# Performance work log

Hardware: AMD Instinct MI355X
Metric: run time of the kernel (lower is better)

Reference implementation:

```python
import jax, jax.numpy as jnp
import numpy as np

EPS = 1e-12


def setup_inputs() -> dict:
    key = jax.random.key(0)
    k1, k2 = jax.random.split(key)
    N, K, D = 32768, 2048, 512
    node_repr = jax.random.normal(k1, (N, D), dtype=jnp.float32)
    mask = jnp.ones((N, 1), dtype=jnp.float32)
    # nn.Embedding weight for the centroids (euclidean branch: exp_map_zero is identity)
    centroid_weight = jax.random.normal(k2, (K, D), dtype=jnp.float32)
    return {"node_repr": node_repr, "mask": mask, "centroid_weight": centroid_weight}


def reference(node_repr, mask, centroid_weight):
    # Euclidean manifold: exp_map_zero(x) = x; distance(x, y) = ||x - y||_2.
    # The torch code expands to [N*K, D]; here we fuse via the Gram-matrix identity
    x2 = jnp.sum(node_repr * node_repr, axis=-1, keepdims=True)        # [N, 1]
    c2 = jnp.sum(centroid_weight * centroid_weight, axis=-1)           # [K]
    xc = jnp.einsum('nd,kd->nk', node_repr, centroid_weight)           # [N, K] GEMM
    d2 = x2 + c2[None, :] - 2.0 * xc                                   # [N, K]
    dist = jnp.sqrt(jnp.maximum(d2, EPS))                              # [N, K]
    node_centroid_dist = dist[None, :, :] * mask[None, :, :]           # [1, N, K] (mask broadcasts [1,N,1])
    graph_centroid_dist = jnp.sum(node_centroid_dist, axis=1) / jnp.sum(mask)  # [1, K]
    return graph_centroid_dist, node_centroid_dist
```

## Files before the change

kernel.cpp:

```cpp
#include <hip/hip_runtime.h>
#include <hip/hip_bf16.h>
#include <math.h>

typedef __bf16 bf16_t;
typedef __bf16 bf16x4 __attribute__((ext_vector_type(4)));
typedef __bf16 bf16x8 __attribute__((ext_vector_type(8)));
typedef float floatx4 __attribute__((ext_vector_type(4)));

#define N_NODES 32768
#define K_CENT  2048
#define D_DIM   512

__global__ void prep_rows_kernel(const float* __restrict__ src,
                                 bf16_t* __restrict__ dst,
                                 float* __restrict__ sq) {
  const int w = threadIdx.x >> 6;
  const int l = threadIdx.x & 63;
  const int row = blockIdx.x * 4 + w;
  const float4* s = (const float4*)(src + (size_t)row * D_DIM);
  float4 f0 = s[l];
  float4 f1 = s[64 + l];
  bf16x4 b0 = { (bf16_t)f0.x, (bf16_t)f0.y, (bf16_t)f0.z, (bf16_t)f0.w };
  bf16x4 b1 = { (bf16_t)f1.x, (bf16_t)f1.y, (bf16_t)f1.z, (bf16_t)f1.w };
  bf16x4* d = (bf16x4*)(dst + (size_t)row * D_DIM);
  d[l] = b0;
  d[64 + l] = b1;
  float v = f0.x*f0.x + f0.y*f0.y + f0.z*f0.z + f0.w*f0.w
          + f1.x*f1.x + f1.y*f1.y + f1.z*f1.z + f1.w*f1.w;
  #pragma unroll
  for (int s2 = 32; s2; s2 >>= 1) v += __shfl_xor(v, s2);
  if (l == 0) sq[row] = v;
}

__global__ void mask_sum_kernel(const float* __restrict__ m,
                                float* __restrict__ out, int n) {
  float v = 0.f;
  for (int i = blockIdx.x * blockDim.x + threadIdx.x; i < n;
       i += gridDim.x * blockDim.x)
    v += m[i];
  #pragma unroll
  for (int s = 32; s; s >>= 1) v += __shfl_xor(v, s);
  __shared__ float red[4];
  if ((threadIdx.x & 63) == 0) red[threadIdx.x >> 6] = v;
  __syncthreads();
  if (threadIdx.x == 0) atomicAdd(out, red[0] + red[1] + red[2] + red[3]);
}

__device__ inline void gld_lds16(const void* g, void* l) {
  __builtin_amdgcn_global_load_lds(
      (__attribute__((address_space(1))) void*)const_cast<void*>(g),
      (__attribute__((address_space(3))) void*)l, 16, 0, 0);
}

__global__ void __launch_bounds__(256)
gemm_dist_kernel(const bf16_t* __restrict__ A,
                 const bf16_t* __restrict__ B,
                 const float* __restrict__ x2,
                 const float* __restrict__ c2,
                 const float* __restrict__ mask,
                 float* __restrict__ out_node,
                 float* __restrict__ colsum) {
  __shared__ __align__(16) bf16_t sA[128 * 64];
  __shared__ __align__(16) bf16_t sB[128 * 64];

  const int t = threadIdx.x;
  const int w = t >> 6;
  const int l = t & 63;

  const int wg = (blockIdx.x & 7) * 512 + (blockIdx.x >> 3);
  const int bm = wg >> 4;
  const int bn = wg & 15;

  const int wm = (w >> 1) * 64;
  const int wn = (w & 1) * 64;
  const int lr = l & 15;
  const int hi = l >> 4;

  floatx4 acc[4][4] = {};

  const int srow = w * 8 + (l >> 3);
  const int scol = ((l & 7) ^ (l >> 3)) * 8;
  const bf16_t* gA = A + (size_t)(bm * 128 + srow) * D_DIM + scol;
  const bf16_t* gB = B + (size_t)(bn * 128 + srow) * D_DIM + scol;
  char* lA = (char*)sA + w * 1024;
  char* lB = (char*)sB + w * 1024;

  for (int kt = 0; kt < D_DIM; kt += 64) {
    #pragma unroll
    for (int p = 0; p < 4; ++p) {
      gld_lds16(gA + (size_t)(p * 32) * D_DIM + kt, lA + p * 4096);
      gld_lds16(gB + (size_t)(p * 32) * D_DIM + kt, lB + p * 4096);
    }
    __syncthreads();
    #pragma unroll
    for (int ks = 0; ks < 2; ++ks) {
      bf16x8 af[4], bfr[4];
      #pragma unroll
      for (int i = 0; i < 4; ++i) {
        const int r = wm + i * 16 + lr;
        const int c = ((ks * 4 + hi) ^ (lr & 7)) * 16;
        af[i] = *(const bf16x8*)((const char*)sA + r * 128 + c);
      }
      #pragma unroll
      for (int j = 0; j < 4; ++j) {
        const int r = wn + j * 16 + lr;
        const int c = ((ks * 4 + hi) ^ (lr & 7)) * 16;
        bfr[j] = *(const bf16x8*)((const char*)sB + r * 128 + c);
      }
      #pragma unroll
      for (int i = 0; i < 4; ++i) {
        #pragma unroll
        for (int j = 0; j < 4; ++j)
          acc[i][j] = __builtin_amdgcn_mfma_f32_16x16x32_bf16(
              af[i], bfr[j], acc[i][j], 0, 0, 0);
      }
    }
    __syncthreads();
  }

  const int col0 = bn * 128 + wn;
  float c2v[4];
  #pragma unroll
  for (int j = 0; j < 4; ++j) c2v[j] = c2[col0 + j * 16 + lr];

  float colacc[4] = {0.f, 0.f, 0.f, 0.f};
  #pragma unroll
  for (int i = 0; i < 4; ++i) {
    const int rbase = bm * 128 + wm + i * 16 + hi * 4;
    #pragma unroll
    for (int r = 0; r < 4; ++r) {
      const int row = rbase + r;
      const float xv = x2[row];
      const float mk = mask[row];
      float* orow = out_node + (size_t)row * K_CENT + col0 + lr;
      #pragma unroll
      for (int j = 0; j < 4; ++j) {
        float d2 = xv + c2v[j] - 2.0f * acc[i][j][r];
        float dist = sqrtf(fmaxf(d2, 1e-12f));
        float dm = dist * mk;
        orow[j * 16] = dm;
        colacc[j] += dm;
      }
    }
  }

  #pragma unroll
  for (int j = 0; j < 4; ++j) {
    colacc[j] += __shfl_xor(colacc[j], 16);
    colacc[j] += __shfl_xor(colacc[j], 32);
  }
  float* colbuf = (float*)sA;
  if (w < 2 && l < 16) {
    #pragma unroll
    for (int j = 0; j < 4; ++j) colbuf[wn + j * 16 + l] = colacc[j];
  }
  __syncthreads();
  if (w >= 2 && l < 16) {
    #pragma unroll
    for (int j = 0; j < 4; ++j) colbuf[wn + j * 16 + l] += colacc[j];
  }
  __syncthreads();
  if (t < 128) atomicAdd(&colsum[bn * 128 + t], colbuf[t]);
}

__global__ void finalize_kernel(const float* __restrict__ colsum,
                                const float* __restrict__ msum,
                                float* __restrict__ out) {
  int k = blockIdx.x * 256 + threadIdx.x;
  out[k] = colsum[k] / msum[0];
}

extern "C" void kernel_launch(void* const* d_in, const int* in_sizes, int n_in,
                              void* d_out, int out_size, void* d_ws, size_t ws_size,
                              hipStream_t stream) {
  const float* node = (const float*)d_in[0];
  const float* mask = (const float*)d_in[1];
  const float* cent = (const float*)d_in[2];
  float* out_graph = (float*)d_out;
  float* out_node  = out_graph + K_CENT;

  char* ws = (char*)d_ws;
  size_t off = 0;
  bf16_t* Abf = (bf16_t*)(ws + off); off += (size_t)N_NODES * D_DIM * sizeof(bf16_t);
  bf16_t* Cbf = (bf16_t*)(ws + off); off += (size_t)K_CENT * D_DIM * sizeof(bf16_t);
  float* x2     = (float*)(ws + off); off += (size_t)N_NODES * sizeof(float);
  float* c2     = (float*)(ws + off); off += (size_t)K_CENT * sizeof(float);
  float* colsum = (float*)(ws + off); off += (size_t)K_CENT * sizeof(float);
  float* msum   = (float*)(ws + off); off += sizeof(float);

  hipMemsetAsync(colsum, 0, (K_CENT + 1) * sizeof(float), stream);

  prep_rows_kernel<<<N_NODES / 4, 256, 0, stream>>>(node, Abf, x2);
  prep_rows_kernel<<<K_CENT / 4, 256, 0, stream>>>(cent, Cbf, c2);
  mask_sum_kernel<<<64, 256, 0, stream>>>(mask, msum, N_NODES);
  gemm_dist_kernel<<<4096, 256, 0, stream>>>(
      Abf, Cbf, x2, c2, mask, out_node, colsum);
  finalize_kernel<<<K_CENT / 256, 256, 0, stream>>>(colsum, msum, out_graph);
}
```

Before: 415.7 us.

## Load GEMM operands directly from global into registers, dropping LDS staging

The GEMM main loop no longer stages A and B tiles through shared memory with global_load_lds and barriers. Each lane now loads its MFMA fragments straight from global memory (fully unrolled over K), and launch bounds request 3 blocks per CU. This removes the LDS traffic and the per-tile __syncthreads, but it loses data reuse across waves, so each tile is fetched from global/L2 twice. Register pressure from the unrolled loads may also rise.

```diff
diff --git a/kernel.cpp b/kernel.cpp
--- a/kernel.cpp
+++ b/kernel.cpp
@@ -46,13 +46,7 @@
   if (threadIdx.x == 0) atomicAdd(out, red[0] + red[1] + red[2] + red[3]);
 }
 
-__device__ inline void gld_lds16(const void* g, void* l) {
-  __builtin_amdgcn_global_load_lds(
-      (__attribute__((address_space(1))) void*)const_cast<void*>(g),
-      (__attribute__((address_space(3))) void*)l, 16, 0, 0);
-}
-
-__global__ void __launch_bounds__(256)
+__global__ void __launch_bounds__(256, 3)
 gemm_dist_kernel(const bf16_t* __restrict__ A,
                  const bf16_t* __restrict__ B,
                  const float* __restrict__ x2,
@@ -60,12 +54,13 @@
                  const float* __restrict__ mask,
                  float* __restrict__ out_node,
                  float* __restrict__ colsum) {
-  __shared__ __align__(16) bf16_t sA[128 * 64];
-  __shared__ __align__(16) bf16_t sB[128 * 64];
+  __shared__ float colbuf[128];
 
   const int t = threadIdx.x;
   const int w = t >> 6;
   const int l = t & 63;
+  const int lr = l & 15;
+  const int hi = l >> 4;
 
   const int wg = (blockIdx.x & 7) * 512 + (blockIdx.x >> 3);
   const int bm = wg >> 4;
@@ -73,49 +68,32 @@
 
   const int wm = (w >> 1) * 64;
   const int wn = (w & 1) * 64;
-  const int lr = l & 15;
-  const int hi = l >> 4;
 
   floatx4 acc[4][4] = {};
 
-  const int srow = w * 8 + (l >> 3);
-  const int scol = ((l & 7) ^ (l >> 3)) * 8;
-  const bf16_t* gA = A + (size_t)(bm * 128 + srow) * D_DIM + scol;
-  const bf16_t* gB = B + (size_t)(bn * 128 + srow) * D_DIM + scol;
-  char* lA = (char*)sA + w * 1024;
-  char* lB = (char*)sB + w * 1024;
+  const bf16_t* aP[4];
+  const bf16_t* bP[4];
+  #pragma unroll
+  for (int i = 0; i < 4; ++i)
+    aP[i] = A + (size_t)(bm * 128 + wm + i * 16 + lr) * D_DIM + hi * 8;
+  #pragma unroll
+  for (int j = 0; j < 4; ++j)
+    bP[j] = B + (size_t)(bn * 128 + wn + j * 16 + lr) * D_DIM + hi * 8;
 
-  for (int kt = 0; kt < D_DIM; kt += 64) {
+  #pragma unroll
+  for (int s = 0; s < 16; ++s) {
+    bf16x8 af[4], bfr[4];
     #pragma unroll
-    for (int p = 0; p < 4; ++p) {
-      gld_lds16(gA + (size_t)(p * 32) * D_DIM + kt, lA + p * 4096);
-      gld_lds16(gB + (size_t)(p * 32) * D_DIM + kt, lB + p * 4096);
+    for (int i = 0; i < 4; ++i) af[i] = *(const bf16x8*)(aP[i] + s * 32);
+    #pragma unroll
+    for (int j = 0; j < 4; ++j) bfr[j] = *(const bf16x8*)(bP[j] + s * 32);
+    #pragma unroll
+    for (int i = 0; i < 4; ++i) {
+      #pragma unroll
+      for (int j = 0; j < 4; ++j)
+        acc[i][j] = __builtin_amdgcn_mfma_f32_16x16x32_bf16(
+            af[i], bfr[j], acc[i][j], 0, 0, 0);
     }
-    __syncthreads();
-    #pragma unroll
-    for (int ks = 0; ks < 2; ++ks) {
-      bf16x8 af[4], bfr[4];
-      #pragma unroll
-      for (int i = 0; i < 4; ++i) {
-        const int r = wm + i * 16 + lr;
-        const int c = ((ks * 4 + hi) ^ (lr & 7)) * 16;
-        af[i] = *(const bf16x8*)((const char*)sA + r * 128 + c);
-      }
-      #pragma unroll
-      for (int j = 0; j < 4; ++j) {
-        const int r = wn + j * 16 + lr;
-        const int c = ((ks * 4 + hi) ^ (lr & 7)) * 16;
-        bfr[j] = *(const bf16x8*)((const char*)sB + r * 128 + c);
-      }
-      #pragma unroll
-      for (int i = 0; i < 4; ++i) {
-        #pragma unroll
-        for (int j = 0; j < 4; ++j)
-          acc[i][j] = __builtin_amdgcn_mfma_f32_16x16x32_bf16(
-              af[i], bfr[j], acc[i][j], 0, 0, 0);
-      }
-    }
-    __syncthreads();
   }
 
   const int col0 = bn * 128 + wn;
@@ -149,7 +127,6 @@
     colacc[j] += __shfl_xor(colacc[j], 16);
     colacc[j] += __shfl_xor(colacc[j], 32);
   }
-  float* colbuf = (float*)sA;
   if (w < 2 && l < 16) {
     #pragma unroll
     for (int j = 0; j < 4; ++j) colbuf[wn + j * 16 + l] = colacc[j];
```

Result: slower. 538.3 us (+29.5%).
